# Kernel tuning notes

Measured on AMD Instinct MI355X. Metric: run time of the kernel, lower is better.

## Reference

```python
import jax, jax.numpy as jnp
import numpy as np
import math

B, T, D = 2, 512, 1024
H, HD = 16, 64
F = 4096
L = 2
R = 32
LOOP_DIM = 64
TEMB = 256
MAXIT = 8
TOPK = 0.55
EPS = 1e-6


def _ste(x, q):
    # straight-through estimator: forward = q, backward = identity
    return x + jax.lax.stop_gradient(q - x)


def bitlinear(x, w, topk_ratio=None):
    # BitNet b1.58 fake-quant: ternary weights (per-tensor absmean scale),
    # int8 per-token absmax activations; optional topk activation sparsity.
    s = jnp.mean(jnp.abs(w)) + 1e-8
    wq = _ste(w, jnp.clip(jnp.round(w / s), -1.0, 1.0) * s)
    if topk_ratio is not None:
        k = max(1, int(math.ceil(topk_ratio * x.shape[-1])))
        ax = jnp.abs(x)
        thr = jax.lax.top_k(ax, k)[0][..., -1:]
        x = jnp.where(ax >= thr, x, 0.0)
    a = jnp.maximum(jnp.max(jnp.abs(x), axis=-1, keepdims=True), 1e-8)
    xq = _ste(x, jnp.clip(jnp.round(x * (127.0 / a)), -128.0, 127.0) * (a / 127.0))
    return xq @ wq.T


def rmsnorm(x, w):
    return x * jax.lax.rsqrt(jnp.mean(x * x, axis=-1, keepdims=True) + EPS) * w


def _rope(x):
    # x: (B,H,T,HD)
    half = HD // 2
    inv = 1.0 / (10000.0 ** (jnp.arange(half, dtype=jnp.float32) / half))
    ang = jnp.arange(x.shape[2], dtype=jnp.float32)[:, None] * inv[None, :]
    cos, sin = jnp.cos(ang), jnp.sin(ang)
    x1, x2 = x[..., :half], x[..., half:]
    return jnp.concatenate([x1 * cos - x2 * sin, x1 * sin + x2 * cos], axis=-1)


def bitblock(h, n1, wq, wk, wv, wo, n2, wg, wu, wd):
    # pre-norm attention + SwiGLU FFN, all projections BitLinear
    b, t, _ = h.shape
    a_in = rmsnorm(h, n1)
    heads = lambda p: p.reshape(b, t, H, HD).transpose(0, 2, 1, 3)
    q = _rope(heads(bitlinear(a_in, wq)))
    k = _rope(heads(bitlinear(a_in, wk)))
    v = heads(bitlinear(a_in, wv))
    scores = jnp.einsum('bhqd,bhkd->bhqk', q, k) / math.sqrt(HD)
    mask = jnp.tril(jnp.ones((t, t), dtype=bool))
    attn = jax.nn.softmax(jnp.where(mask, scores, -1e9), axis=-1)
    o = jnp.einsum('bhqk,bhkd->bhqd', attn, v).transpose(0, 2, 1, 3).reshape(b, t, D)
    h = h + bitlinear(o, wo)
    f_in = rmsnorm(h, n2)
    h = h + bitlinear(jax.nn.silu(bitlinear(f_in, wg)) * bitlinear(f_in, wu), wd)
    return h


def loop_delta(i, t_emb, lp_w, lp2_w, lp2_b):
    # loop_index_inject: sinusoidal loop signal gated by t_emb, padded to D
    half = LOOP_DIM // 2
    frac = i / max(MAXIT - 1, 1)
    freqs = jnp.exp(-math.log(10000.0) * jnp.arange(half, dtype=jnp.float32) / half)
    ang = frac * freqs
    sig = jnp.concatenate([jnp.sin(ang), jnp.cos(ang)])  # (LOOP_DIM,)
    comb = sig[None, :] * (t_emb @ lp_w.T) + (t_emb @ lp2_w.T + lp2_b)  # (B,LOOP_DIM)
    return jnp.pad(comb, ((0, 0), (0, D - LOOP_DIM)))[:, None, :]  # (B,1,D)


def setup_inputs() -> dict:
    key = jax.random.key(0)
    ks = jax.random.split(key, 24)
    g = lambda k, shape, sc=0.02: sc * jax.random.normal(k, shape, dtype=jnp.float32)
    return {
        'x': jax.random.normal(ks[0], (B, T, D), dtype=jnp.float32),
        'e': jax.random.normal(ks[1], (B, T, D), dtype=jnp.float32),
        't_emb': jax.random.normal(ks[2], (B, TEMB), dtype=jnp.float32),
        'blk_norm1': jnp.ones((L, D), jnp.float32),
        'blk_wq': g(ks[3], (L, D, D)),
        'blk_wk': g(ks[4], (L, D, D)),
        'blk_wv': g(ks[5], (L, D, D)),
        'blk_wo': g(ks[6], (L, D, D)),
        'blk_norm2': jnp.ones((L, D), jnp.float32),
        'blk_wg': g(ks[7], (L, F, D)),
        'blk_wu': g(ks[8], (L, F, D)),
        'blk_wd': g(ks[9], (L, D, F)),
        'A_raw': 0.1 * jax.random.normal(ks[10], (D,), dtype=jnp.float32),
        'B_w': g(ks[11], (D, D)),
        'lora_down': g(ks[12], (R, D)),
        'lora_up': g(ks[13], (D, R)),
        'iter_gate': jnp.full((MAXIT,), 0.1, jnp.float32),
        'act_w': g(ks[14], (1, D)),
        'alpha': jnp.full((MAXIT,), 1.0 / L, jnp.float32),
        'loop_proj_w': g(ks[15], (LOOP_DIM, TEMB)),
        'loop_proj2_w': g(ks[16], (LOOP_DIM, TEMB)),
        'loop_proj2_b': jnp.zeros((LOOP_DIM,), jnp.float32),
        'loop_norm_w': jnp.ones((D,), jnp.float32),
        'n_loops': 8,
    }


def reference(x, e, t_emb, blk_norm1, blk_wq, blk_wk, blk_wv, blk_wo,
              blk_norm2, blk_wg, blk_wu, blk_wd, A_raw, B_w,
              lora_down, lora_up, iter_gate, act_w, alpha,
              loop_proj_w, loop_proj2_w, loop_proj2_b, loop_norm_w, n_loops):
    A_eff = 0.99 * jnp.tanh(A_raw)          # diagonal LTI, |A|<0.99
    Be = bitlinear(e, B_w)                  # loop-invariant anchor B(e)
    h = x
    h_out = x
    ws = []
    for i in range(int(n_loops)):
        h_in = rmsnorm(h + loop_delta(i, t_emb, loop_proj_w, loop_proj2_w, loop_proj2_b), loop_norm_w)
        bo = h_in
        for l in range(L):
            bo = bitblock(bo, blk_norm1[l], blk_wq[l], blk_wk[l], blk_wv[l], blk_wo[l],
                          blk_norm2[l], blk_wg[l], blk_wu[l], blk_wd[l])
        bo = alpha[i] * bo
        h = A_eff * h + Be + bo             # LTI injection
        h = h + iter_gate[i] * bitlinear(bitlinear(h, lora_down), lora_up, topk_ratio=TOPK)
        w = jax.nn.sigmoid(bitlinear(h, act_w))  # (B,T,1) soft ACT weight
        h_out = h_out + w * (h - h_out)     # incremental residual blend
        ws.append(w)
    ponder = jnp.mean(jnp.stack(ws))
    return h_out, ponder
```

## Files before the change

kernel.cpp:

```cpp
#include <hip/hip_runtime.h>
#include <stdint.h>

#define DEV static __device__ __forceinline__

typedef float f32x4 __attribute__((ext_vector_type(4)));
typedef int   i32x4 __attribute__((ext_vector_type(4)));
typedef unsigned short u16x8 __attribute__((ext_vector_type(8)));

DEV float bf2f(unsigned short u){ return __uint_as_float(((unsigned int)u)<<16); }
DEV unsigned short f2bfr(float f){
  unsigned int u = __float_as_uint(f);
  return (unsigned short)((u + 0x7FFF + ((u>>16)&1)) >> 16);
}
DEV signed char f2i8(float f){ return (signed char)(int)f; }

DEV float wredsum(float v){
#pragma unroll
  for (int o=32;o;o>>=1) v += __shfl_xor(v,o);
  return v;
}
DEV float wredmax(float v){
#pragma unroll
  for (int o=32;o;o>>=1) v = fmaxf(v,__shfl_xor(v,o));
  return v;
}
DEV float bredsum(float v, float* red){
  v = wredsum(v);
  if ((threadIdx.x&63)==0) red[threadIdx.x>>6] = v;
  __syncthreads();
  float r = red[0]+red[1]+red[2]+red[3];
  __syncthreads();
  return r;
}
DEV float bredmax(float v, float* red){
  v = wredmax(v);
  if ((threadIdx.x&63)==0) red[threadIdx.x>>6] = v;
  __syncthreads();
  float r = fmaxf(fmaxf(red[0],red[1]),fmaxf(red[2],red[3]));
  __syncthreads();
  return r;
}

__global__ void fill_k(float* p, int n, float v){
  int i = blockIdx.x*256 + threadIdx.x;
  if (i < n) p[i] = v;
}

__global__ __launch_bounds__(256) void setup_misc_k(const float* __restrict__ x,
                                                    float* __restrict__ h, float* __restrict__ ho,
                                                    const float* __restrict__ temb,
                                                    const float* __restrict__ lpw,
                                                    const float* __restrict__ lp2w,
                                                    const float* __restrict__ lp2b,
                                                    float* __restrict__ delta,
                                                    float* __restrict__ tab){
  __shared__ float red[4];
  int bid = blockIdx.x, t = threadIdx.x;
  if (bid < 1024){
    int i = bid*256 + t;
    float4 v = *(const float4*)(x + (size_t)i*4);
    *(float4*)(h  + (size_t)i*4) = v;
    *(float4*)(ho + (size_t)i*4) = v;
    if (i==0) ho[1048576] = 0.f;
  } else if (bid < 1152){
    int blk = bid - 1024;
    int b = blk >> 6, j = blk & 63;
    float te = temb[b*256 + t];
    float p1 = bredsum(te * lpw[j*256 + t], red);
    float p2 = bredsum(te * lp2w[j*256 + t], red);
    if (t < 8){
      int i = t;
      float frac = (float)i / 7.f;
      int jj = j & 31;
      float fr = expf(-logf(10000.f) * (float)jj * (1.f/32.f));
      float ang = frac * fr;
      float sig = (j < 32) ? sinf(ang) : cosf(ang);
      delta[i*128 + b*64 + j] = sig*p1 + p2 + lp2b[j];
    }
  } else {
    int i = (bid-1152)*256 + t;
    int tpos = i >> 5, d = i & 31;
    float inv = powf(10000.f, -(float)d * (1.f/32.f));
    float sv, cv; sincosf((float)tpos * inv, &sv, &cv);
    tab[i*2]   = cv;
    tab[i*2+1] = sv;
  }
}

struct WSetup {
  const float* src[18];
  signed char* dst[18];
  int mode[18];
};
DEV long n4of(int mat){ return mat<9 ? 262144 : (mat<15 ? 1048576 : (mat<17 ? 8192 : 256)); }

__global__ __launch_bounds__(256) void absmean_all_k(WSetup wsu, float* __restrict__ part){
  __shared__ float red[4];
  int mat = blockIdx.x >> 8;
  int seg = blockIdx.x & 255;
  long n4 = n4of(mat);
  long cnt = n4 >> 8;
  const float4* p = (const float4*)wsu.src[mat] + (long)seg*cnt;
  float s0=0.f, s1=0.f, s2=0.f, s3=0.f;
  if (cnt >= 1024){
    long quar = cnt >> 2;
    const float4* p1 = p + quar;
    const float4* p2 = p + 2*quar;
    const float4* p3 = p + 3*quar;
#pragma unroll 2
    for (long j = threadIdx.x; j < quar; j += 256){
      float4 a = p[j], b = p1[j], c = p2[j], d = p3[j];
      s0 += fabsf(a.x)+fabsf(a.y)+fabsf(a.z)+fabsf(a.w);
      s1 += fabsf(b.x)+fabsf(b.y)+fabsf(b.z)+fabsf(b.w);
      s2 += fabsf(c.x)+fabsf(c.y)+fabsf(c.z)+fabsf(c.w);
      s3 += fabsf(d.x)+fabsf(d.y)+fabsf(d.z)+fabsf(d.w);
    }
  } else {
    for (long j = threadIdx.x; j < cnt; j += 256){
      float4 a = p[j];
      s0 += fabsf(a.x)+fabsf(a.y)+fabsf(a.z)+fabsf(a.w);
    }
  }
  float s = bredsum(s0+s1+s2+s3, red);
  if (threadIdx.x==0) part[(long)mat*256 + seg] = s;
}

__global__ __launch_bounds__(256) void finalize_scales_k(const float* __restrict__ part,
                                                         float* __restrict__ scales){
  __shared__ float red[4];
  const long numel[18] = {1048576, 1048576,1048576, 1048576,1048576, 1048576,1048576,
                          1048576,1048576, 4194304,4194304, 4194304,4194304, 4194304,4194304,
                          32768, 32768, 1024};
  for (int m=0;m<18;m++){
    float v = part[(long)m*256 + threadIdx.x];
    v = bredsum(v, red);
    if (threadIdx.x==0) scales[m] = v/(float)numel[m] + 1e-8f;
  }
  if (threadIdx.x==0){
    for (int l=0;l<2;l++){
      scales[18+l*3+0] = scales[1+l];
      scales[18+l*3+1] = scales[3+l];
      scales[18+l*3+2] = scales[5+l];
      scales[24+l*2+0] = scales[9+l];
      scales[24+l*2+1] = scales[11+l];
    }
  }
}

__global__ __launch_bounds__(256) void quantw_all_k(WSetup wsu, const float* __restrict__ scales){
  int bid = blockIdx.x;
  int mat = 0, c = 0;
  for (;;){
    int nb = mat<9 ? 256 : (mat<15 ? 1024 : (mat<17 ? 8 : 1));
    if (bid < c + nb) break;
    c += nb; mat++;
  }
  long seg = bid - c;
  long n4 = n4of(mat);
  float s = scales[mat];
  int md = wsu.mode[mat];
  const float4* src = (const float4*)wsu.src[mat];
  char4* dst = (char4*)wsu.dst[mat];
  long base = seg*1024;
#pragma unroll
  for (int k=0;k<4;k++){
    long i = base + k*256 + threadIdx.x;
    if (i < n4){
      float4 v = src[i];
      char4 q;
      q.x = f2i8(fminf(fmaxf(rintf(v.x/s), -1.f), 1.f));
      q.y = f2i8(fminf(fmaxf(rintf(v.y/s), -1.f), 1.f));
      q.z = f2i8(fminf(fmaxf(rintf(v.z/s), -1.f), 1.f));
      q.w = f2i8(fminf(fmaxf(rintf(v.w/s), -1.f), 1.f));
      if (md == 0) dst[i] = q;
      else {
        long r = i >> 8, cc = i & 255;
        dst[(((r<<1) | (md-1))<<8) | cc] = q;
      }
    }
  }
}

template<bool BF>
__global__ __launch_bounds__(256) void rowquant1k_k(const void* __restrict__ xin,
                                                    signed char* __restrict__ xq,
                                                    float* __restrict__ rs){
  __shared__ float red[4];
  int m = blockIdx.x, t = threadIdx.x;
  float v[4];
  if (BF){
    ushort4 u = *(const ushort4*)((const unsigned short*)xin + (size_t)m*1024 + t*4);
    v[0]=bf2f(u.x); v[1]=bf2f(u.y); v[2]=bf2f(u.z); v[3]=bf2f(u.w);
  } else {
    float4 f = *(const float4*)((const float*)xin + (size_t)m*1024 + t*4);
    v[0]=f.x; v[1]=f.y; v[2]=f.z; v[3]=f.w;
  }
  float am = fmaxf(fmaxf(fabsf(v[0]),fabsf(v[1])),fmaxf(fabsf(v[2]),fabsf(v[3])));
  am = bredmax(am, red);
  float a = fmaxf(am, 1e-8f), inv = 127.f/a;
  char4 q;
  q.x = f2i8(fminf(fmaxf(rintf(v[0]*inv),-128.f),127.f));
  q.y = f2i8(fminf(fmaxf(rintf(v[1]*inv),-128.f),127.f));
  q.z = f2i8(fminf(fmaxf(rintf(v[2]*inv),-128.f),127.f));
  q.w = f2i8(fminf(fmaxf(rintf(v[3]*inv),-128.f),127.f));
  *(char4*)(xq + (size_t)m*1024 + t*4) = q;
  if (t==0) rs[m] = a/127.f;
}

__global__ __launch_bounds__(256) void rowquant4k_k(const unsigned short* __restrict__ x,
                                                    signed char* __restrict__ xq,
                                                    float* __restrict__ rs){
  __shared__ float red[4];
  int m = blockIdx.x, t = threadIdx.x;
  const unsigned short* p = x + (size_t)m*4096 + t*16;
  u16x8 u0 = *(const u16x8*)p;
  u16x8 u1 = *(const u16x8*)(p + 8);
  float v[16];
#pragma unroll
  for (int j=0;j<8;j++){ v[j] = bf2f(u0[j]); v[j+8] = bf2f(u1[j]); }
  float am = 0.f;
#pragma unroll
  for (int j=0;j<16;j++) am = fmaxf(am, fabsf(v[j]));
  am = bredmax(am, red);
  float a = fmaxf(am, 1e-8f), inv = 127.f/a;
#pragma unroll
  for (int j=0;j<16;j+=4){
    char4 q;
    q.x = f2i8(fminf(fmaxf(rintf(v[j+0]*inv),-128.f),127.f));
    q.y = f2i8(fminf(fmaxf(rintf(v[j+1]*inv),-128.f),127.f));
    q.z = f2i8(fminf(fmaxf(rintf(v[j+2]*inv),-128.f),127.f));
    q.w = f2i8(fminf(fmaxf(rintf(v[j+3]*inv),-128.f),127.f));
    *(char4*)(xq + (size_t)m*4096 + t*16 + j) = q;
  }
  if (t==0) rs[m] = a/127.f;
}

__global__ __launch_bounds__(256) void loopnorm_quant_k(const float* __restrict__ h,
                                                        const float* __restrict__ delta,
                                                        const float* __restrict__ lnw,
                                                        const float* __restrict__ n1,
                                                        float* __restrict__ hin,
                                                        signed char* __restrict__ xq,
                                                        float* __restrict__ rs){
  __shared__ float red[4];
  int m = blockIdx.x, t = threadIdx.x;
  int b = m >> 9;
  float v[4];
  float4 f = *(const float4*)(h + (size_t)m*1024 + t*4);
  v[0]=f.x; v[1]=f.y; v[2]=f.z; v[3]=f.w;
  if (t < 16){
#pragma unroll
    for (int j=0;j<4;j++) v[j] += delta[b*64 + t*4 + j];
  }
  float ss = v[0]*v[0]+v[1]*v[1]+v[2]*v[2]+v[3]*v[3];
  ss = bredsum(ss, red);
  float r1 = rsqrtf(ss*(1.f/1024.f) + 1e-6f);
  float w4[4];
#pragma unroll
  for (int j=0;j<4;j++) w4[j] = v[j]*r1*lnw[t*4+j];
  float4 of; of.x=w4[0]; of.y=w4[1]; of.z=w4[2]; of.w=w4[3];
  *(float4*)(hin + (size_t)m*1024 + t*4) = of;
  float s2 = w4[0]*w4[0]+w4[1]*w4[1]+w4[2]*w4[2]+w4[3]*w4[3];
  s2 = bredsum(s2, red);
  float r2 = rsqrtf(s2*(1.f/1024.f) + 1e-6f);
  float y[4];
#pragma unroll
  for (int j=0;j<4;j++) y[j] = w4[j]*r2*n1[t*4+j];
  float am = fmaxf(fmaxf(fabsf(y[0]),fabsf(y[1])),fmaxf(fabsf(y[2]),fabsf(y[3])));
  am = bredmax(am, red);
  float a = fmaxf(am, 1e-8f), inv = 127.f/a;
  char4 q;
  q.x = f2i8(fminf(fmaxf(rintf(y[0]*inv),-128.f),127.f));
  q.y = f2i8(fminf(fmaxf(rintf(y[1]*inv),-128.f),127.f));
  q.z = f2i8(fminf(fmaxf(rintf(y[2]*inv),-128.f),127.f));
  q.w = f2i8(fminf(fmaxf(rintf(y[3]*inv),-128.f),127.f));
  *(char4*)(xq + (size_t)m*1024 + t*4) = q;
  if (t==0) rs[m] = a/127.f;
}

DEV f32x4 accfence(f32x4 c){ asm volatile("s_nop 7\n\ts_nop 7" : "+v"(c)); return c; }
DEV i32x4 accfencei(i32x4 c){ asm volatile("s_nop 7\n\ts_nop 7" : "+v"(c)); return c; }

template<bool SPLITK, bool GUSILU>
__global__ __launch_bounds__(256)
void gemm_i8(const signed char* __restrict__ A, const signed char* __restrict__ W,
             const float* __restrict__ rowsc, const float* __restrict__ wscv,
             const float* __restrict__ res, float* __restrict__ C, int N, int Kf, int Kc)
{
  __shared__ __align__(16) signed char As[2][8192];
  __shared__ __align__(16) signed char Bs[2][8192];
  const int tid = threadIdx.x;
  const int lane = tid & 63, wvid = tid >> 6;
  const int wr = wvid >> 1, wc = wvid & 1;
  const int bm = blockIdx.y, bn = blockIdx.x;

  const int r0 = (wvid<<4) + (lane>>2);
  const int sw = (((lane&3) ^ ((r0>>1)&3)) << 4);
  const long kstart = SPLITK ? (long)blockIdx.z * Kc : 0;
  const signed char* gA = A + (size_t)(bm*128 + r0)*Kf + kstart + sw;
  const signed char* gB = W + (size_t)(bn*128 + r0)*Kf + kstart + sw;
  const size_t row64 = (size_t)64*Kf;

#define STAGE(buf, koff) do { \
    __builtin_amdgcn_global_load_lds(gA + (koff),         &As[buf][(wvid<<10)],      16, 0, 0); \
    __builtin_amdgcn_global_load_lds(gA + (koff) + row64, &As[buf][(wvid<<10)+4096], 16, 0, 0); \
    __builtin_amdgcn_global_load_lds(gB + (koff),         &Bs[buf][(wvid<<10)],      16, 0, 0); \
    __builtin_amdgcn_global_load_lds(gB + (koff) + row64, &Bs[buf][(wvid<<10)+4096], 16, 0, 0); \
  } while(0)

  i32x4 acc[4][4] = {};
  const int rA = (wr<<6) + (lane&15);
  const int rB = (wc<<6) + (lane&15);
  const int psA = (((lane>>4) ^ (((lane&15)>>1)&3)) << 4);

  STAGE(0, 0);
  const int NT = Kc >> 6;
  int cur = 0;
  for (int kt = 0; kt < NT; ++kt){
    const int knext = (kt+1 < NT) ? ((kt+1)<<6) : 0;
    STAGE(cur^1, knext);
    asm volatile("s_waitcnt vmcnt(4)" ::: "memory");
    __builtin_amdgcn_s_barrier();
    asm volatile("" ::: "memory");
    i32x4 a[4], b[4];
    const signed char* Ab = As[cur];
    const signed char* Bb = Bs[cur];
#pragma unroll
    for (int mi=0;mi<4;mi++) a[mi] = *(const i32x4*)(Ab + (rA + mi*16)*64 + psA);
#pragma unroll
    for (int ni=0;ni<4;ni++) b[ni] = *(const i32x4*)(Bb + (rB + ni*16)*64 + psA);
#pragma unroll
    for (int mi=0;mi<4;mi++)
#pragma unroll
      for (int ni=0;ni<4;ni++)
        asm("v_mfma_i32_16x16x64_i8 %0, %1, %2, %0" : "+v"(acc[mi][ni]) : "v"(a[mi]), "v"(b[ni]));
    asm volatile("s_waitcnt lgkmcnt(0)" ::: "memory");
    __builtin_amdgcn_s_barrier();
    cur ^= 1;
  }
#undef STAGE

#pragma unroll
  for (int mi=0;mi<4;mi++)
#pragma unroll
    for (int ni=0;ni<4;ni++)
      acc[mi][ni] = accfencei(acc[mi][ni]);

  const int rif = (lane>>4)<<2;
  const int cif = lane&15;
  const int gcol0 = bn*128 + (wc<<6);

  if constexpr (SPLITK){
    float* P = C + (size_t)blockIdx.z * ((size_t)N << 10);
#pragma unroll
    for (int mi=0;mi<4;mi++)
#pragma unroll
      for (int r=0;r<4;r++){
        const int grow = bm*128 + (wr<<6) + mi*16 + rif + r;
#pragma unroll
        for (int ni=0;ni<4;ni++)
          P[(size_t)grow*N + gcol0 + ni*16 + cif] = (float)acc[mi][ni][r];
      }
    return;
  }

  if constexpr (GUSILU){
    const float sg = wscv[0], su = wscv[1];
    unsigned short* Cb = (unsigned short*)C;
#pragma unroll
    for (int mi=0;mi<4;mi++){
#pragma unroll
      for (int r=0;r<4;r++){
        const int grow = bm*128 + (wr<<6) + mi*16 + rif + r;
        const float rsc = rowsc[grow];
#pragma unroll
        for (int ni=0;ni<4;ni++){
          const int gcol = gcol0 + ni*16 + cif;
          float val = (float)acc[mi][ni][r] * rsc * ((gcol & 1) ? su : sg);
          float other = __shfl_xor(val, 1);
          if (!(lane & 1)){
            float g = val, u = other;
            float outv = g/(1.f+expf(-g))*u;
            Cb[(size_t)grow*4096 + (gcol>>1)] = f2bfr(outv);
          }
        }
      }
    }
    return;
  }

#pragma unroll
  for (int mi=0;mi<4;mi++){
#pragma unroll
    for (int r=0;r<4;r++){
      const int grow = bm*128 + (wr<<6) + mi*16 + rif + r;
      const float rsc = rowsc[grow];
#pragma unroll
      for (int ni=0;ni<4;ni++){
        const int gcol = gcol0 + ni*16 + cif;
        float vvv = (float)acc[mi][ni][r] * rsc * wscv[0];
        const size_t off = (size_t)grow*N + gcol;
        if (res) vvv += res[off];
        C[off] = vvv;
      }
    }
  }
}

__global__ __launch_bounds__(256)
void gemm_qkv128(const signed char* __restrict__ A, const signed char* __restrict__ W,
                 const float* __restrict__ rowsc, const float* __restrict__ wscv,
                 const float* __restrict__ tab, unsigned short* __restrict__ C)
{
  __shared__ __align__(16) signed char As[2][8192];
  __shared__ __align__(16) signed char Bs[2][8192];
  const int tid = threadIdx.x;
  const int lane = tid & 63, wvid = tid >> 6;
  const int wr = wvid >> 1, wc = wvid & 1;
  const int bm = blockIdx.y, bn = blockIdx.x;
  const int Kf = 1024;

  const int r0 = (wvid<<4) + (lane>>2);
  const int sw = (((lane&3) ^ ((r0>>1)&3)) << 4);
  const signed char* gA = A + (size_t)(bm*128 + r0)*Kf + sw;
  const signed char* gB = W + (size_t)(bn*128 + r0)*Kf + sw;
  const size_t row64 = (size_t)64*Kf;

#define STAGE(buf, koff) do { \
    __builtin_amdgcn_global_load_lds(gA + (koff),         &As[buf][(wvid<<10)],      16, 0, 0); \
    __builtin_amdgcn_global_load_lds(gA + (koff) + row64, &As[buf][(wvid<<10)+4096], 16, 0, 0); \
    __builtin_amdgcn_global_load_lds(gB + (koff),         &Bs[buf][(wvid<<10)],      16, 0, 0); \
    __builtin_amdgcn_global_load_lds(gB + (koff) + row64, &Bs[buf][(wvid<<10)+4096], 16, 0, 0); \
  } while(0)

  i32x4 acc[4][4] = {};
  const int rA = (wr<<6) + (lane&15);
  const int rB = (wc<<6) + (lane&15);
  const int psA = (((lane>>4) ^ (((lane&15)>>1)&3)) << 4);

  STAGE(0, 0);
  const int NT = 16;
  int cur = 0;
  for (int kt = 0; kt < NT; ++kt){
    const int knext = (kt+1 < NT) ? ((kt+1)<<6) : 0;
    STAGE(cur^1, knext);
    asm volatile("s_waitcnt vmcnt(4)" ::: "memory");
    __builtin_amdgcn_s_barrier();
    asm volatile("" ::: "memory");
    i32x4 a[4], b[4];
    const signed char* Ab = As[cur];
    const signed char* Bb = Bs[cur];
#pragma unroll
    for (int mi=0;mi<4;mi++) a[mi] = *(const i32x4*)(Ab + (rA + mi*16)*64 + psA);
#pragma unroll
    for (int ni=0;ni<4;ni++) b[ni] = *(const i32x4*)(Bb + (rB + ni*16)*64 + psA);
#pragma unroll
    for (int mi=0;mi<4;mi++)
#pragma unroll
      for (int ni=0;ni<4;ni++)
        asm("v_mfma_i32_16x16x64_i8 %0, %1, %2, %0" : "+v"(acc[mi][ni]) : "v"(a[mi]), "v"(b[ni]));
    asm volatile("s_waitcnt lgkmcnt(0)" ::: "memory");
    __builtin_amdgcn_s_barrier();
    cur ^= 1;
  }
#undef STAGE

#pragma unroll
  for (int mi=0;mi<4;mi++)
#pragma unroll
    for (int ni=0;ni<4;ni++)
      acc[mi][ni] = accfencei(acc[mi][ni]);

  const int rif = (lane>>4)<<2;
  const int cif = lane&15;
  const int gcol0 = bn*128 + (wc<<6);
  const int sec = gcol0 >> 10;
  const float wsc = wscv[sec] * ((sec==0) ? 0.125f : 1.f);

  if (sec < 2){
#pragma unroll
    for (int mi=0;mi<4;mi++){
#pragma unroll
      for (int r=0;r<4;r++){
        const int grow = bm*128 + (wr<<6) + mi*16 + rif + r;
        const float s = rowsc[grow] * wsc;
        const int tpos = grow & 511;
#pragma unroll
        for (int np=0;np<2;np++){
          const int d = np*16 + cif;
          float2 cs = *(const float2*)(tab + (size_t)((tpos<<5) + d)*2);
          float x1 = (float)acc[mi][np][r]   * s;
          float x2 = (float)acc[mi][np+2][r] * s;
          C[(size_t)grow*3072 + gcol0 + d]      = f2bfr(x1*cs.x - x2*cs.y);
          C[(size_t)grow*3072 + gcol0 + 32 + d] = f2bfr(x1*cs.y + x2*cs.x);
        }
      }
    }
  } else {
#pragma unroll
    for (int mi=0;mi<4;mi++){
#pragma unroll
      for (int r=0;r<4;r++){
        const int grow = bm*128 + (wr<<6) + mi*16 + rif + r;
        const float s = rowsc[grow] * wsc;
#pragma unroll
        for (int ni=0;ni<4;ni++)
          C[(size_t)grow*3072 + gcol0 + ni*16 + cif] = f2bfr((float)acc[mi][ni][r] * s);
      }
    }
  }
}

__global__ __launch_bounds__(256) void reduce4_k(const float* __restrict__ P,
                                                 const float* __restrict__ rowsc,
                                                 const float* __restrict__ wsc,
                                                 const float* __restrict__ res,
                                                 float* __restrict__ C){
  int m = blockIdx.x, t = threadIdx.x;
  float s0 = rowsc[m] * wsc[0];
  size_t off = (size_t)m*1024 + t*4;
  float4 a = *(const float4*)(P + off);
  float4 b = *(const float4*)(P + 1048576 + off);
  float4 c = *(const float4*)(P + 2097152 + off);
  float4 d = *(const float4*)(P + 3145728 + off);
  float4 o;
  o.x = (a.x+b.x+c.x+d.x)*s0;
  o.y = (a.y+b.y+c.y+d.y)*s0;
  o.z = (a.z+b.z+c.z+d.z)*s0;
  o.w = (a.w+b.w+c.w+d.w)*s0;
  if (res){
    float4 r = *(const float4*)(res + off);
    o.x += r.x; o.y += r.y; o.z += r.z; o.w += r.w;
  }
  *(float4*)(C + off) = o;
}

__global__ __launch_bounds__(256) void redq_norm_k(const float* __restrict__ P,
                                                   const float* rowsc,
                                                   const float* __restrict__ wsc,
                                                   const float* __restrict__ res,
                                                   const float* __restrict__ gamma,
                                                   float* __restrict__ Cout,
                                                   signed char* __restrict__ xq,
                                                   float* rs){
  __shared__ float red[4];
  int m = blockIdx.x, t = threadIdx.x;
  float s0 = rowsc[m] * wsc[0];
  size_t off = (size_t)m*1024 + t*4;
  float4 a = *(const float4*)(P + off);
  float4 b = *(const float4*)(P + 1048576 + off);
  float4 c = *(const float4*)(P + 2097152 + off);
  float4 d = *(const float4*)(P + 3145728 + off);
  float4 r4 = *(const float4*)(res + off);
  float v[4];
  v[0] = r4.x + (a.x+b.x+c.x+d.x)*s0;
  v[1] = r4.y + (a.y+b.y+c.y+d.y)*s0;
  v[2] = r4.z + (a.z+b.z+c.z+d.z)*s0;
  v[3] = r4.w + (a.w+b.w+c.w+d.w)*s0;
  float4 of; of.x=v[0]; of.y=v[1]; of.z=v[2]; of.w=v[3];
  *(float4*)(Cout + off) = of;
  float ss = v[0]*v[0]+v[1]*v[1]+v[2]*v[2]+v[3]*v[3];
  ss = bredsum(ss, red);
  float r1 = rsqrtf(ss*(1.f/1024.f) + 1e-6f);
  float y[4];
#pragma unroll
  for (int j=0;j<4;j++) y[j] = v[j]*r1*gamma[t*4+j];
  float am = fmaxf(fmaxf(fabsf(y[0]),fabsf(y[1])),fmaxf(fabsf(y[2]),fabsf(y[3])));
  am = bredmax(am, red);
  float aq = fmaxf(am, 1e-8f), inv = 127.f/aq;
  char4 q;
  q.x = f2i8(fminf(fmaxf(rintf(y[0]*inv),-128.f),127.f));
  q.y = f2i8(fminf(fmaxf(rintf(y[1]*inv),-128.f),127.f));
  q.z = f2i8(fminf(fmaxf(rintf(y[2]*inv),-128.f),127.f));
  q.w = f2i8(fminf(fmaxf(rintf(y[3]*inv),-128.f),127.f));
  *(char4*)(xq + (size_t)m*1024 + t*4) = q;
  if (t==0) rs[m] = aq/127.f;
}

__global__ __launch_bounds__(256) void redfin_k(const float* __restrict__ P,
                                                const float* __restrict__ rowsc,
                                                const float* __restrict__ wsc,
                                                const float* __restrict__ res,
                                                float* __restrict__ h,
                                                const float* __restrict__ Be,
                                                const float* __restrict__ Araw,
                                                const float* __restrict__ alpha, int it,
                                                const signed char* __restrict__ ldq,
                                                const float* __restrict__ sld,
                                                const signed char* __restrict__ luq,
                                                const float* __restrict__ slu,
                                                const signed char* __restrict__ actq,
                                                const float* __restrict__ sact,
                                                const float* __restrict__ ig,
                                                float* __restrict__ hout,
                                                float* __restrict__ ponder,
                                                const float* __restrict__ dnext,
                                                const float* __restrict__ lnw,
                                                const float* __restrict__ n1,
                                                float* __restrict__ hin,
                                                signed char* __restrict__ xqn,
                                                float* __restrict__ rsn,
                                                int doNext){
  __shared__ float red[4];
  __shared__ float xrow[1024];
  __shared__ float part[256];
  __shared__ float xs[32];
  __shared__ float sh_thr, sh_gs;
  int m = blockIdx.x, t = threadIdx.x;
  float al = alpha[it];
  float s0 = rowsc[m] * wsc[0];
  size_t off = (size_t)m*1024 + t*4;
  float4 a = *(const float4*)(P + off);
  float4 b = *(const float4*)(P + 1048576 + off);
  float4 c = *(const float4*)(P + 2097152 + off);
  float4 d = *(const float4*)(P + 3145728 + off);
  float4 r4 = *(const float4*)(res + off);
  float4 hh = *(const float4*)(h + off);
  float4 be = *(const float4*)(Be + off);
  float4 ar = *(const float4*)(Araw + t*4);
  float v[4];
  v[0] = 0.99f*tanhf(ar.x)*hh.x + be.x + al*(r4.x + (a.x+b.x+c.x+d.x)*s0);
  v[1] = 0.99f*tanhf(ar.y)*hh.y + be.y + al*(r4.y + (a.y+b.y+c.y+d.y)*s0);
  v[2] = 0.99f*tanhf(ar.z)*hh.z + be.z + al*(r4.z + (a.z+b.z+c.z+d.z)*s0);
  v[3] = 0.99f*tanhf(ar.w)*hh.w + be.w + al*(r4.w + (a.w+b.w+c.w+d.w)*s0);
  float am = fmaxf(fmaxf(fabsf(v[0]),fabsf(v[1])),fmaxf(fabsf(v[2]),fabsf(v[3])));
  am = bredmax(am, red);
  float aq = fmaxf(am, 1e-8f), inv = 127.f/aq;
#pragma unroll
  for (int j=0;j<4;j++) xrow[t*4+j] = fminf(fmaxf(rintf(v[j]*inv),-128.f),127.f);
  float rsv = aq/127.f;
  __syncthreads();
  {
    int r = t & 31, seg = t >> 5;
    const signed char* wrow = ldq + (size_t)r*1024 + seg*128;
    const float* xr = xrow + seg*128;
    float acc = 0.f;
    for (int k=0;k<128;k+=4){
      char4 w4 = *(const char4*)(wrow + k);
      acc += xr[k]*(float)w4.x + xr[k+1]*(float)w4.y + xr[k+2]*(float)w4.z + xr[k+3]*(float)w4.w;
    }
    part[t] = acc;
  }
  __syncthreads();
  if (t < 32){
    float s = 0.f;
    for (int sg=0; sg<8; sg++) s += part[sg*32 + t];
    xs[t] = s * rsv * (*sld);
  }
  __syncthreads();
  float val = 0.f, av = 0.f, amax = 0.f;
  if (t < 32){
    val = xs[t]; av = fabsf(val);
    int rank = 0;
    for (int j=0;j<32;j++){
      float aj = fabsf(xs[j]);
      amax = fmaxf(amax, aj);
      if (aj > av || (aj == av && j < t)) rank++;
    }
    if (rank == 17) sh_thr = av;
  }
  __syncthreads();
  if (t < 32){
    float a2 = fmaxf(amax, 1e-8f);
    float q = 0.f;
    if (av >= sh_thr) q = fminf(fmaxf(rintf(val*(127.f/a2)), -128.f), 127.f);
    xs[t] = q;
    if (t == 0) sh_gs = ig[it] * (*slu) * (a2/127.f);
  }
  __syncthreads();
  float gs = sh_gs;
  float hn[4];
  int n0 = t*4;
#pragma unroll
  for (int ni=0;ni<4;ni++){
    const signed char* lr = luq + (size_t)(n0+ni)*32;
    float dd = 0.f;
    for (int k=0;k<32;k+=4){
      char4 w4 = *(const char4*)(lr + k);
      dd += xs[k]*(float)w4.x + xs[k+1]*(float)w4.y + xs[k+2]*(float)w4.z + xs[k+3]*(float)w4.w;
    }
    hn[ni] = v[ni] + gs*dd;
  }
  float am2 = fmaxf(fmaxf(fabsf(hn[0]),fabsf(hn[1])),fmaxf(fabsf(hn[2]),fabsf(hn[3])));
  am2 = bredmax(am2, red);
  float a2 = fmaxf(am2, 1e-8f), inv2 = 127.f/a2;
  float zp = 0.f;
#pragma unroll
  for (int ni=0;ni<4;ni++){
    float q = fminf(fmaxf(rintf(hn[ni]*inv2),-128.f),127.f);
    zp += q * (float)actq[n0+ni];
  }
  zp = bredsum(zp, red);
  float z = zp * (a2/127.f) * (*sact);
  float wv = 1.f/(1.f+expf(-z));
#pragma unroll
  for (int ni=0;ni<4;ni++){
    size_t o2 = (size_t)m*1024 + n0+ni;
    float ho = hout[o2];
    hout[o2] = ho + wv*(hn[ni]-ho);
    h[o2] = hn[ni];
  }
  if (t==0) atomicAdd(ponder, wv * (1.f/8192.f));

  if (doNext){
    int b2 = m >> 9;
    float v2[4] = {hn[0], hn[1], hn[2], hn[3]};
    if (t < 16){
#pragma unroll
      for (int j=0;j<4;j++) v2[j] += dnext[b2*64 + t*4 + j];
    }
    float ss2 = v2[0]*v2[0]+v2[1]*v2[1]+v2[2]*v2[2]+v2[3]*v2[3];
    ss2 = bredsum(ss2, red);
    float r1 = rsqrtf(ss2*(1.f/1024.f) + 1e-6f);
    float w4[4];
#pragma unroll
    for (int j=0;j<4;j++) w4[j] = v2[j]*r1*lnw[t*4+j];
    float4 of; of.x=w4[0]; of.y=w4[1]; of.z=w4[2]; of.w=w4[3];
    *(float4*)(hin + off) = of;
    float s2 = w4[0]*w4[0]+w4[1]*w4[1]+w4[2]*w4[2]+w4[3]*w4[3];
    s2 = bredsum(s2, red);
    float r2 = rsqrtf(s2*(1.f/1024.f) + 1e-6f);
    float y[4];
#pragma unroll
    for (int j=0;j<4;j++) y[j] = w4[j]*r2*n1[t*4+j];
    float am3 = fmaxf(fmaxf(fabsf(y[0]),fabsf(y[1])),fmaxf(fabsf(y[2]),fabsf(y[3])));
    am3 = bredmax(am3, red);
    float aq3 = fmaxf(am3, 1e-8f), inv3 = 127.f/aq3;
    char4 q;
    q.x = f2i8(fminf(fmaxf(rintf(y[0]*inv3),-128.f),127.f));
    q.y = f2i8(fminf(fmaxf(rintf(y[1]*inv3),-128.f),127.f));
    q.z = f2i8(fminf(fmaxf(rintf(y[2]*inv3),-128.f),127.f));
    q.w = f2i8(fminf(fmaxf(rintf(y[3]*inv3),-128.f),127.f));
    *(char4*)(xqn + off) = q;
    if (t==0) rsn[m] = aq3/127.f;
  }
}

DEV int swz64(int r, int c){ return r*64 + (c ^ ((r&7)<<3)); }

__global__ __launch_bounds__(256) void attn_bf16_k(const unsigned short* __restrict__ qkv,
                                                   unsigned short* __restrict__ o){
  __shared__ __align__(16) unsigned short Qs[4096];
  __shared__ __align__(16) unsigned short Ks[4096];
  __shared__ __align__(16) unsigned short Vt[4096];
  __shared__ __align__(16) unsigned short Ps[4][1024];
  const int tid = threadIdx.x;
  const int lane = tid & 63, wv = tid >> 6;
  const int qt = blockIdx.x & 7, bh = blockIdx.x >> 3;
  const int b = bh >> 4, h = bh & 15;
  const int tokb = b*512;
  const int l15 = lane & 15, lh = lane >> 4;

  {
    int r = tid >> 2, c0 = (tid & 3) << 4;
    const unsigned short* s = qkv + (size_t)(tokb + qt*64 + r)*3072 + h*64 + c0;
    u16x8 f0 = *(const u16x8*)s, f1 = *(const u16x8*)(s+8);
    *(u16x8*)(Qs + swz64(r, c0))   = f0;
    *(u16x8*)(Qs + swz64(r, c0+8)) = f1;
  }

  float m_run[4] = {-1e30f,-1e30f,-1e30f,-1e30f};
  float l_run[4] = {0.f,0.f,0.f,0.f};
  f32x4 accO[4] = {};

  for (int kt = 0; kt <= qt; ++kt){
    __syncthreads();
    {
      int r = tid >> 2, c0 = (tid & 3) << 4;
      const unsigned short* s = qkv + (size_t)(tokb + kt*64 + r)*3072 + 1024 + h*64 + c0;
      u16x8 f0 = *(const u16x8*)s, f1 = *(const u16x8*)(s+8);
      *(u16x8*)(Ks + swz64(r, c0))   = f0;
      *(u16x8*)(Ks + swz64(r, c0+8)) = f1;
    }
    {
      int r0 = (tid >> 3) << 1, cv = (tid & 7) << 3;
      const unsigned short* s0 = qkv + (size_t)(tokb + kt*64 + r0)*3072 + 2048 + h*64 + cv;
      u16x8 a = *(const u16x8*)s0;
      u16x8 b2 = *(const u16x8*)(s0 + 3072);
#pragma unroll
      for (int j=0;j<8;j++){
        int d = cv + j;
        unsigned int pk = (unsigned int)a[j] | ((unsigned int)b2[j]<<16);
        *(unsigned int*)(Vt + swz64(d, r0)) = pk;
      }
    }
    __syncthreads();

    f32x4 s4[4] = {};
#pragma unroll
    for (int kc=0; kc<2; ++kc){
      i32x4 aq = *(const i32x4*)(Qs + swz64(wv*16 + l15, kc*32 + lh*8));
#pragma unroll
      for (int nt=0; nt<4; ++nt){
        i32x4 bk = *(const i32x4*)(Ks + swz64(nt*16 + l15, kc*32 + lh*8));
        asm("v_mfma_f32_16x16x32_bf16 %0, %1, %2, %0" : "+v"(s4[nt]) : "v"(aq), "v"(bk));
      }
    }
#pragma unroll
    for (int nt=0; nt<4; ++nt) s4[nt] = accfence(s4[nt]);

    const bool diag = (kt == qt);
    float sf[4];
#pragma unroll
    for (int r=0;r<4;r++){
      int rl = lh*4 + r;
      float mx = -1e30f;
#pragma unroll
      for (int nt=0; nt<4; ++nt){
        float v = s4[nt][r];
        if (diag && (nt*16 + l15) > (wv*16 + rl)) v = -1e30f;
        s4[nt][r] = v;
        mx = fmaxf(mx, v);
      }
      mx = fmaxf(mx, __shfl_xor(mx,1));
      mx = fmaxf(mx, __shfl_xor(mx,2));
      mx = fmaxf(mx, __shfl_xor(mx,4));
      mx = fmaxf(mx, __shfl_xor(mx,8));
      float mn = fmaxf(m_run[r], mx);
      sf[r] = __expf(m_run[r] - mn);
      m_run[r] = mn;
      float ps = 0.f;
#pragma unroll
      for (int nt=0; nt<4; ++nt){
        float p = __expf(s4[nt][r] - mn);
        ps += p;
        Ps[wv][swz64(rl, nt*16 + l15)] = f2bfr(p);
      }
      ps += __shfl_xor(ps,1); ps += __shfl_xor(ps,2);
      ps += __shfl_xor(ps,4); ps += __shfl_xor(ps,8);
      l_run[r] = l_run[r]*sf[r] + ps;
    }
#pragma unroll
    for (int dt=0; dt<4; ++dt){
#pragma unroll
      for (int r=0;r<4;r++) accO[dt][r] *= sf[r];
      accO[dt] = accfence(accO[dt]);
    }
#pragma unroll
    for (int kc=0; kc<2; ++kc){
      i32x4 pa = *(const i32x4*)(Ps[wv] + swz64(l15, kc*32 + lh*8));
#pragma unroll
      for (int dt=0; dt<4; ++dt){
        i32x4 vb3 = *(const i32x4*)(Vt + swz64(dt*16 + l15, kc*32 + lh*8));
        asm("v_mfma_f32_16x16x32_bf16 %0, %1, %2, %0" : "+v"(accO[dt]) : "v"(pa), "v"(vb3));
      }
    }
  }
#pragma unroll
  for (int dt=0; dt<4; ++dt) accO[dt] = accfence(accO[dt]);
#pragma unroll
  for (int r=0;r<4;r++){
    float invl = 1.f / l_run[r];
    int row = qt*64 + wv*16 + lh*4 + r;
    unsigned short* op = o + (size_t)(tokb + row)*1024 + h*64 + l15;
#pragma unroll
    for (int dt=0; dt<4; ++dt)
      op[dt*16] = f2bfr(accO[dt][r] * invl);
  }
}

extern "C" void kernel_launch(void* const* d_in, const int* in_sizes, int n_in,
                              void* d_out, int out_size, void* d_ws, size_t ws_size,
                              hipStream_t stream)
{
  (void)in_sizes; (void)n_in;
  const float* x     = (const float*)d_in[0];
  const float* e     = (const float*)d_in[1];
  const float* temb  = (const float*)d_in[2];
  const float* bn1   = (const float*)d_in[3];
  const float* bwq   = (const float*)d_in[4];
  const float* bwk   = (const float*)d_in[5];
  const float* bwv   = (const float*)d_in[6];
  const float* bwo   = (const float*)d_in[7];
  const float* bn2   = (const float*)d_in[8];
  const float* bwg   = (const float*)d_in[9];
  const float* bwu   = (const float*)d_in[10];
  const float* bwd   = (const float*)d_in[11];
  const float* Araw  = (const float*)d_in[12];
  const float* Bw    = (const float*)d_in[13];
  const float* ldw   = (const float*)d_in[14];
  const float* luw   = (const float*)d_in[15];
  const float* ig    = (const float*)d_in[16];
  const float* actw  = (const float*)d_in[17];
  const float* alph  = (const float*)d_in[18];
  const float* lpw   = (const float*)d_in[19];
  const float* lp2w  = (const float*)d_in[20];
  const float* lp2b  = (const float*)d_in[21];
  const float* lnw   = (const float*)d_in[22];

  char* ws = (char*)d_ws;
  float* out = (float*)d_out;
  const size_t WS_NEEDED = 94600704ull;
  if (ws_size < WS_NEEDED){
    fill_k<<<(out_size+255)/256,256,0,stream>>>(out, out_size, 1.0e9f);
    return;
  }

  signed char* qw_qkv = (signed char*)(ws + 0);
  signed char* qw_wo  = (signed char*)(ws + 6291456);
  signed char* qw_gu  = (signed char*)(ws + 8388608);
  signed char* qw_wd  = (signed char*)(ws + 25165824);
  signed char* qw_bw  = (signed char*)(ws + 33554432);
  signed char* qw_ld  = (signed char*)(ws + 34603008);
  signed char* qw_lu  = (signed char*)(ws + 34635776);
  signed char* qw_act = (signed char*)(ws + 34668544);
  float* scales = (float*)(ws + 34669568);
  float* part   = (float*)(ws + 34670080);
  float* delta  = (float*)(ws + 34688512);
  float* hbuf   = (float*)(ws + 34692608);
  float* Bebuf  = (float*)(ws + 38886912);
  float* bufX   = (float*)(ws + 43081216);
  float* bufY   = (float*)(ws + 47275520);
  float* gub    = (float*)(ws + 51469824);
  unsigned short* qkv_bf = (unsigned short*)(ws + 76635648);
  unsigned short* obuf = (unsigned short*)(ws + 85024256);
  signed char* xq1k = (signed char*)(ws + 89218560);
  float* rs1k   = (float*)(ws + 90267136);
  signed char* xqm  = (signed char*)(ws + 90271232);
  float* rsm    = (float*)(ws + 94465536);
  float* ropetab= (float*)(ws + 94469632);

  WSetup wsu;
  wsu.src[0]=Bw;
  wsu.src[1]=bwq; wsu.src[2]=bwq+1048576;
  wsu.src[3]=bwk; wsu.src[4]=bwk+1048576;
  wsu.src[5]=bwv; wsu.src[6]=bwv+1048576;
  wsu.src[7]=bwo; wsu.src[8]=bwo+1048576;
  wsu.src[9]=bwg; wsu.src[10]=bwg+4194304;
  wsu.src[11]=bwu; wsu.src[12]=bwu+4194304;
  wsu.src[13]=bwd; wsu.src[14]=bwd+4194304;
  wsu.src[15]=ldw; wsu.src[16]=luw; wsu.src[17]=actw;
  wsu.dst[0]=qw_bw;
  wsu.dst[1]=qw_qkv;             wsu.dst[2]=qw_qkv+3145728;
  wsu.dst[3]=qw_qkv+1048576;     wsu.dst[4]=qw_qkv+3145728+1048576;
  wsu.dst[5]=qw_qkv+2097152;     wsu.dst[6]=qw_qkv+3145728+2097152;
  wsu.dst[7]=qw_wo;              wsu.dst[8]=qw_wo+1048576;
  wsu.dst[9]=qw_gu;              wsu.dst[10]=qw_gu+8388608;
  wsu.dst[11]=qw_gu;             wsu.dst[12]=qw_gu+8388608;
  wsu.dst[13]=qw_wd;             wsu.dst[14]=qw_wd+4194304;
  wsu.dst[15]=qw_ld; wsu.dst[16]=qw_lu; wsu.dst[17]=qw_act;
  for (int i=0;i<18;i++) wsu.mode[i]=0;
  wsu.mode[9]=1;  wsu.mode[10]=1;
  wsu.mode[11]=2; wsu.mode[12]=2;

  absmean_all_k<<<4608,256,0,stream>>>(wsu, part);
  finalize_scales_k<<<1,256,0,stream>>>(part, scales);
  quantw_all_k<<<8465,256,0,stream>>>(wsu, scales);

  setup_misc_k<<<1216,256,0,stream>>>(x, hbuf, out, temb, lpw, lp2w, lp2b, delta, ropetab);

  rowquant1k_k<false><<<1024,256,0,stream>>>(e, xq1k, rs1k);
  { dim3 g(8,8,4); gemm_i8<true,false><<<g,256,0,stream>>>(xq1k, qw_bw, nullptr, nullptr, nullptr, gub, 1024, 1024, 256); }
  reduce4_k<<<1024,256,0,stream>>>(gub, rs1k, scales+0, nullptr, Bebuf);

  for (int it=0; it<8; ++it){
    if (it==0)
      loopnorm_quant_k<<<1024,256,0,stream>>>(hbuf, delta, lnw, bn1, bufX, xq1k, rs1k);
    for (int l=0;l<2;l++){
      { dim3 g(24,8); gemm_qkv128<<<g,256,0,stream>>>(xq1k, qw_qkv + (size_t)l*3145728, rs1k, scales+18+l*3, ropetab, qkv_bf); }
      attn_bf16_k<<<256,256,0,stream>>>(qkv_bf, obuf);
      rowquant1k_k<true><<<1024,256,0,stream>>>(obuf, xq1k, rs1k);
      { dim3 g(8,8,4); gemm_i8<true,false><<<g,256,0,stream>>>(xq1k, qw_wo + (size_t)l*1048576, nullptr, nullptr, nullptr, gub, 1024, 1024, 256); }
      redq_norm_k<<<1024,256,0,stream>>>(gub, rs1k, scales+7+l, bufX, bn2 + (size_t)l*1024, bufY, xq1k, rs1k);
      { dim3 g(64,8); gemm_i8<false,true><<<g,256,0,stream>>>(xq1k, qw_gu + (size_t)l*8388608, rs1k, scales+24+l*2, nullptr, gub, 8192, 1024, 1024); }
      rowquant4k_k<<<1024,256,0,stream>>>((const unsigned short*)gub, xqm, rsm);
      { dim3 g(8,8,4); gemm_i8<true,false><<<g,256,0,stream>>>(xqm, qw_wd + (size_t)l*4194304, nullptr, nullptr, nullptr, gub, 1024, 4096, 1024); }
      if (l==0){
        redq_norm_k<<<1024,256,0,stream>>>(gub, rsm, scales+13, bufY, bn1 + 1024, bufX, xq1k, rs1k);
      } else {
        redfin_k<<<1024,256,0,stream>>>(gub, rsm, scales+14, bufY, hbuf, Bebuf, Araw, alph, it,
                                        qw_ld, scales+15, qw_lu, scales+16, qw_act, scales+17,
                                        ig, out, out + 1048576,
                                        delta + (it+1 < 8 ? (it+1)*128 : 0), lnw, bn1, bufX, xq1k, rs1k,
                                        (it < 7) ? 1 : 0);
      }
    }
  }
}
```

Measured before the change: 1.989 ms.

## Triple-buffer int8 GEMM LDS staging and widen absmean partial-sum grid

Both int8 GEMM kernels move from double to triple LDS buffering, prefetching two K-tiles ahead and waiting with vmcnt(8), so more global-load latency can be hidden behind MFMA work. Separately, the absmean reduction now splits the large FFN matrices into 1024 segments instead of 256, giving more blocks for parallelism, and finalize sums the variable number of partials. The partials buffer is moved onto the gub scratch region to fit the larger size. LDS use per block grows by half, which may lower occupancy.

```diff
diff --git a/kernel.cpp b/kernel.cpp
--- a/kernel.cpp
+++ b/kernel.cpp
@@ -96,10 +96,13 @@
 
 __global__ __launch_bounds__(256) void absmean_all_k(WSetup wsu, float* __restrict__ part){
   __shared__ float red[4];
-  int mat = blockIdx.x >> 8;
-  int seg = blockIdx.x & 255;
+  int bid = blockIdx.x, mat, seg;
+  if (bid < 2304){ mat = bid >> 8; seg = bid & 255; }
+  else if (bid < 8448){ mat = 9 + ((bid-2304) >> 10); seg = (bid-2304) & 1023; }
+  else { mat = 15 + ((bid-8448) >> 8); seg = (bid-8448) & 255; }
   long n4 = n4of(mat);
-  long cnt = n4 >> 8;
+  int segs = (mat >= 9 && mat < 15) ? 1024 : 256;
+  long cnt = n4 / segs;
   const float4* p = (const float4*)wsu.src[mat] + (long)seg*cnt;
   float s0=0.f, s1=0.f, s2=0.f, s3=0.f;
   if (cnt >= 1024){
@@ -107,7 +110,6 @@
     const float4* p1 = p + quar;
     const float4* p2 = p + 2*quar;
     const float4* p3 = p + 3*quar;
-#pragma unroll 2
     for (long j = threadIdx.x; j < quar; j += 256){
       float4 a = p[j], b = p1[j], c = p2[j], d = p3[j];
       s0 += fabsf(a.x)+fabsf(a.y)+fabsf(a.z)+fabsf(a.w);
@@ -122,7 +124,7 @@
     }
   }
   float s = bredsum(s0+s1+s2+s3, red);
-  if (threadIdx.x==0) part[(long)mat*256 + seg] = s;
+  if (threadIdx.x==0) part[(long)mat*1024 + seg] = s;
 }
 
 __global__ __launch_bounds__(256) void finalize_scales_k(const float* __restrict__ part,
@@ -131,12 +133,15 @@
   const long numel[18] = {1048576, 1048576,1048576, 1048576,1048576, 1048576,1048576,
                           1048576,1048576, 4194304,4194304, 4194304,4194304, 4194304,4194304,
                           32768, 32768, 1024};
+  int t = threadIdx.x;
   for (int m=0;m<18;m++){
-    float v = part[(long)m*256 + threadIdx.x];
+    int segs = (m >= 9 && m < 15) ? 1024 : 256;
+    float v = 0.f;
+    for (int j=t; j<segs; j+=256) v += part[(long)m*1024 + j];
     v = bredsum(v, red);
-    if (threadIdx.x==0) scales[m] = v/(float)numel[m] + 1e-8f;
-  }
-  if (threadIdx.x==0){
+    if (t==0) scales[m] = v/(float)numel[m] + 1e-8f;
+  }
+  if (t==0){
     for (int l=0;l<2;l++){
       scales[18+l*3+0] = scales[1+l];
       scales[18+l*3+1] = scales[3+l];
@@ -287,8 +292,8 @@
              const float* __restrict__ rowsc, const float* __restrict__ wscv,
              const float* __restrict__ res, float* __restrict__ C, int N, int Kf, int Kc)
 {
-  __shared__ __align__(16) signed char As[2][8192];
-  __shared__ __align__(16) signed char Bs[2][8192];
+  __shared__ __align__(16) signed char As[3][8192];
+  __shared__ __align__(16) signed char Bs[3][8192];
   const int tid = threadIdx.x;
   const int lane = tid & 63, wvid = tid >> 6;
   const int wr = wvid >> 1, wc = wvid & 1;
@@ -313,13 +318,15 @@
   const int rB = (wc<<6) + (lane&15);
   const int psA = (((lane>>4) ^ (((lane&15)>>1)&3)) << 4);
 
+  const int NT = Kc >> 6;
   STAGE(0, 0);
-  const int NT = Kc >> 6;
-  int cur = 0;
+  STAGE(1, 64);
+  int cur = 0, nxt = 1, nx2 = 2;
   for (int kt = 0; kt < NT; ++kt){
-    const int knext = (kt+1 < NT) ? ((kt+1)<<6) : 0;
-    STAGE(cur^1, knext);
-    asm volatile("s_waitcnt vmcnt(4)" ::: "memory");
+    const int k2 = kt + 2;
+    const int kn = (k2 < NT) ? (k2<<6) : 0;
+    STAGE(nx2, kn);
+    asm volatile("s_waitcnt vmcnt(8)" ::: "memory");
     __builtin_amdgcn_s_barrier();
     asm volatile("" ::: "memory");
     i32x4 a[4], b[4];
@@ -336,7 +343,7 @@
         asm("v_mfma_i32_16x16x64_i8 %0, %1, %2, %0" : "+v"(acc[mi][ni]) : "v"(a[mi]), "v"(b[ni]));
     asm volatile("s_waitcnt lgkmcnt(0)" ::: "memory");
     __builtin_amdgcn_s_barrier();
-    cur ^= 1;
+    int tmp = cur; cur = nxt; nxt = nx2; nx2 = tmp;
   }
 #undef STAGE
 
@@ -412,8 +419,8 @@
                  const float* __restrict__ rowsc, const float* __restrict__ wscv,
                  const float* __restrict__ tab, unsigned short* __restrict__ C)
 {
-  __shared__ __align__(16) signed char As[2][8192];
-  __shared__ __align__(16) signed char Bs[2][8192];
+  __shared__ __align__(16) signed char As[3][8192];
+  __shared__ __align__(16) signed char Bs[3][8192];
   const int tid = threadIdx.x;
   const int lane = tid & 63, wvid = tid >> 6;
   const int wr = wvid >> 1, wc = wvid & 1;
@@ -438,13 +445,15 @@
   const int rB = (wc<<6) + (lane&15);
   const int psA = (((lane>>4) ^ (((lane&15)>>1)&3)) << 4);
 
+  const int NT = 16;
   STAGE(0, 0);
-  const int NT = 16;
-  int cur = 0;
+  STAGE(1, 64);
+  int cur = 0, nxt = 1, nx2 = 2;
   for (int kt = 0; kt < NT; ++kt){
-    const int knext = (kt+1 < NT) ? ((kt+1)<<6) : 0;
-    STAGE(cur^1, knext);
-    asm volatile("s_waitcnt vmcnt(4)" ::: "memory");
+    const int k2 = kt + 2;
+    const int kn = (k2 < NT) ? (k2<<6) : 0;
+    STAGE(nx2, kn);
+    asm volatile("s_waitcnt vmcnt(8)" ::: "memory");
     __builtin_amdgcn_s_barrier();
     asm volatile("" ::: "memory");
     i32x4 a[4], b[4];
@@ -461,7 +470,7 @@
         asm("v_mfma_i32_16x16x64_i8 %0, %1, %2, %0" : "+v"(acc[mi][ni]) : "v"(a[mi]), "v"(b[ni]));
     asm volatile("s_waitcnt lgkmcnt(0)" ::: "memory");
     __builtin_amdgcn_s_barrier();
-    cur ^= 1;
+    int tmp = cur; cur = nxt; nxt = nx2; nx2 = tmp;
   }
 #undef STAGE
 
@@ -905,7 +914,6 @@
   signed char* qw_lu  = (signed char*)(ws + 34635776);
   signed char* qw_act = (signed char*)(ws + 34668544);
   float* scales = (float*)(ws + 34669568);
-  float* part   = (float*)(ws + 34670080);
   float* delta  = (float*)(ws + 34688512);
   float* hbuf   = (float*)(ws + 34692608);
   float* Bebuf  = (float*)(ws + 38886912);
@@ -919,6 +927,7 @@
   signed char* xqm  = (signed char*)(ws + 90271232);
   float* rsm    = (float*)(ws + 94465536);
   float* ropetab= (float*)(ws + 94469632);
+  float* part   = gub;
 
   WSetup wsu;
   wsu.src[0]=Bw;
@@ -943,7 +952,7 @@
   wsu.mode[9]=1;  wsu.mode[10]=1;
   wsu.mode[11]=2; wsu.mode[12]=2;
 
-  absmean_all_k<<<4608,256,0,stream>>>(wsu, part);
+  absmean_all_k<<<9216,256,0,stream>>>(wsu, part);
   finalize_scales_k<<<1,256,0,stream>>>(part, scales);
   quantw_all_k<<<8465,256,0,stream>>>(wsu, scales);
 
```

New measurement: 1.965 ms. No clear change (-1.2%).
